# Kernel tuning notes

Hardware: AMD Instinct MI355X
Metric: run time of the kernel (lower is better)

## Reference

```python
import jax, jax.numpy as jnp
import numpy as np

NNZ = 819200
NUM_SESS = 16384
ITEMS_NUM = 1000000
EMB_DIM = 64


def setup_inputs() -> dict:
    key = jax.random.key(0)
    k1, k2, k3, k4 = jax.random.split(key, 4)
    row_idx = jnp.sort(jax.random.randint(k1, (NNZ,), 0, NUM_SESS, dtype=jnp.int32))
    col_idx = jax.random.randint(k2, (NNZ,), 0, ITEMS_NUM, dtype=jnp.int32)
    data_tensor = jax.random.uniform(k3, (NNZ,), dtype=jnp.float32)
    embeddings = jax.random.normal(k4, (ITEMS_NUM, EMB_DIM), dtype=jnp.float32)
    return {
        "row_idx": row_idx,
        "col_idx": col_idx,
        "data_tensor": data_tensor,
        "num_ids": NUM_SESS,
        "embeddings": embeddings,
    }


def reference(row_idx, col_idx, data_tensor, num_ids, embeddings):
    # sparse_coo([num_ids, ITEMS_NUM]) @ embeddings
    # == per-session weighted sum of gathered item embeddings.
    gathered = embeddings[col_idx]                      # [nnz, d]
    weighted = gathered * data_tensor[:, None]          # [nnz, d]
    user_embeddings = jax.ops.segment_sum(
        weighted, row_idx, num_segments=num_ids)        # [num_ids, d]
    return user_embeddings
```

## Files before the change

kernel.cpp:

```cpp
#include <hip/hip_runtime.h>


__global__ __launch_bounds__(256) void build_rowptr_kernel(
    const int* __restrict__ row_idx,
    int*       __restrict__ row_ptr,
    int nnz, int num_sess)
{
    int j = blockIdx.x * blockDim.x + threadIdx.x;
    if (j >= nnz) return;
    int r = row_idx[j];
    if (j == 0) {
        for (int s = 0; s <= r; ++s) row_ptr[s] = 0;
    } else {
        int rp = row_idx[j - 1];
        for (int s = rp + 1; s <= r; ++s) row_ptr[s] = j;
    }
    if (j == nnz - 1) {
        for (int s = r + 1; s <= num_sess; ++s) row_ptr[s] = nnz;
    }
}

__global__ __launch_bounds__(256, 8) void wsum_sess_kernel(
    const int*    __restrict__ row_ptr,
    const int*    __restrict__ col_idx,
    const float*  __restrict__ data,
    const float4* __restrict__ emb,
    float4*       __restrict__ out,
    int num_sess)
{
    const int wave = threadIdx.x >> 6;
    const int lane = threadIdx.x & 63;
    const int sess = (blockIdx.x << 2) + wave;
    if (sess >= num_sess) return;

    const int start = row_ptr[sess];
    const int end   = row_ptr[sess + 1];

    const int r = lane >> 4;
    const int c = lane & 15;

    float4 acc = make_float4(0.f, 0.f, 0.f, 0.f);

    int j0 = start;
    for (; j0 + 16 <= end; j0 += 16) {
        int   c0 = col_idx[j0 + 0  + r];
        int   c1 = col_idx[j0 + 4  + r];
        int   c2 = col_idx[j0 + 8  + r];
        int   c3 = col_idx[j0 + 12 + r];
        float w0 = data[j0 + 0  + r];
        float w1 = data[j0 + 4  + r];
        float w2 = data[j0 + 8  + r];
        float w3 = data[j0 + 12 + r];
        float4 e0 = emb[((size_t)c0 << 4) + c];
        float4 e1 = emb[((size_t)c1 << 4) + c];
        float4 e2 = emb[((size_t)c2 << 4) + c];
        float4 e3 = emb[((size_t)c3 << 4) + c];
        acc.x += w0 * e0.x + w1 * e1.x + w2 * e2.x + w3 * e3.x;
        acc.y += w0 * e0.y + w1 * e1.y + w2 * e2.y + w3 * e3.y;
        acc.z += w0 * e0.z + w1 * e1.z + w2 * e2.z + w3 * e3.z;
        acc.w += w0 * e0.w + w1 * e1.w + w2 * e2.w + w3 * e3.w;
    }
    for (; j0 < end; j0 += 4) {
        int   j     = j0 + r;
        bool  valid = (j < end);
        int   col   = valid ? col_idx[j] : 0;
        float w     = valid ? data[j]    : 0.f;
        float4 e = emb[((size_t)col << 4) + c];
        acc.x += w * e.x;
        acc.y += w * e.y;
        acc.z += w * e.z;
        acc.w += w * e.w;
    }

    acc.x += __shfl_xor(acc.x, 16, 64);
    acc.y += __shfl_xor(acc.y, 16, 64);
    acc.z += __shfl_xor(acc.z, 16, 64);
    acc.w += __shfl_xor(acc.w, 16, 64);
    acc.x += __shfl_xor(acc.x, 32, 64);
    acc.y += __shfl_xor(acc.y, 32, 64);
    acc.z += __shfl_xor(acc.z, 32, 64);
    acc.w += __shfl_xor(acc.w, 32, 64);

    if (r == 0)
        out[((size_t)sess << 4) + c] = acc;
}

extern "C" void kernel_launch(void* const* d_in, const int* in_sizes, int n_in,
                              void* d_out, int out_size, void* d_ws, size_t ws_size,
                              hipStream_t stream) {
    const int*   row_idx = (const int*)  d_in[0];
    const int*   col_idx = (const int*)  d_in[1];
    const float* data    = (const float*)d_in[2];
    const float* emb     = (const float*)d_in[4];

    const int nnz      = in_sizes[0];
    const int num_sess = out_size / 64;

    int* row_ptr = (int*)d_ws;

    build_rowptr_kernel<<<(nnz + 255) / 256, 256, 0, stream>>>(
        row_idx, row_ptr, nnz, num_sess);

    const int blocks = (num_sess + 3) / 4;
    wsum_sess_kernel<<<blocks, 256, 0, stream>>>(
        row_ptr, col_idx, data, (const float4*)emb, (float4*)d_out,
        num_sess);
}
```

Measured before the change: 325.3 us.

## Map one embedding column per lane and broadcast indices via readlane

Restructures the per-session gather so each lane owns one of the 64 embedding dimensions. A wave loads up to 64 col/weight pairs cooperatively and broadcasts each one with readlane. Up to 32 row loads are issued in flight before the accumulation, which removes the cross-lane shuffle reduction. The tradeoffs are scalar float loads instead of float4 loads, and padding work of up to 32 rows for short sessions (about 50 nnz per session on average), which wastes bandwidth on invalid entries that point at row 0.

```diff
diff --git a/kernel.cpp b/kernel.cpp
--- a/kernel.cpp
+++ b/kernel.cpp
@@ -21,11 +21,11 @@
 }
 
 __global__ __launch_bounds__(256, 8) void wsum_sess_kernel(
-    const int*    __restrict__ row_ptr,
-    const int*    __restrict__ col_idx,
-    const float*  __restrict__ data,
-    const float4* __restrict__ emb,
-    float4*       __restrict__ out,
+    const int*   __restrict__ row_ptr,
+    const int*   __restrict__ col_idx,
+    const float* __restrict__ data,
+    const float* __restrict__ emb,
+    float*       __restrict__ out,
     int num_sess)
 {
     const int wave = threadIdx.x >> 6;
@@ -36,53 +36,34 @@
     const int start = row_ptr[sess];
     const int end   = row_ptr[sess + 1];
 
-    const int r = lane >> 4;
-    const int c = lane & 15;
+    float acc = 0.0f;
 
-    float4 acc = make_float4(0.f, 0.f, 0.f, 0.f);
+    for (int j0 = start; j0 < end; j0 += 64) {
+        const int jl    = j0 + lane;
+        const bool valid = (jl < end);
+        int   col = valid ? col_idx[jl] : 0;
+        float w   = valid ? data[jl]    : 0.0f;
+        const int rem = end - j0;
 
-    int j0 = start;
-    for (; j0 + 16 <= end; j0 += 16) {
-        int   c0 = col_idx[j0 + 0  + r];
-        int   c1 = col_idx[j0 + 4  + r];
-        int   c2 = col_idx[j0 + 8  + r];
-        int   c3 = col_idx[j0 + 12 + r];
-        float w0 = data[j0 + 0  + r];
-        float w1 = data[j0 + 4  + r];
-        float w2 = data[j0 + 8  + r];
-        float w3 = data[j0 + 12 + r];
-        float4 e0 = emb[((size_t)c0 << 4) + c];
-        float4 e1 = emb[((size_t)c1 << 4) + c];
-        float4 e2 = emb[((size_t)c2 << 4) + c];
-        float4 e3 = emb[((size_t)c3 << 4) + c];
-        acc.x += w0 * e0.x + w1 * e1.x + w2 * e2.x + w3 * e3.x;
-        acc.y += w0 * e0.y + w1 * e1.y + w2 * e2.y + w3 * e3.y;
-        acc.z += w0 * e0.z + w1 * e1.z + w2 * e2.z + w3 * e3.z;
-        acc.w += w0 * e0.w + w1 * e1.w + w2 * e2.w + w3 * e3.w;
-    }
-    for (; j0 < end; j0 += 4) {
-        int   j     = j0 + r;
-        bool  valid = (j < end);
-        int   col   = valid ? col_idx[j] : 0;
-        float w     = valid ? data[j]    : 0.f;
-        float4 e = emb[((size_t)col << 4) + c];
-        acc.x += w * e.x;
-        acc.y += w * e.y;
-        acc.z += w * e.z;
-        acc.w += w * e.w;
+        #pragma unroll
+        for (int kb = 0; kb < 64; kb += 32) {
+            if (kb >= rem) break;
+            float v[32];
+            float wk[32];
+            #pragma unroll
+            for (int k = 0; k < 32; ++k) {
+                int c = __builtin_amdgcn_readlane(col, kb + k);
+                wk[k] = __int_as_float(
+                            __builtin_amdgcn_readlane(__float_as_int(w), kb + k));
+                v[k] = emb[(size_t)c * 64 + lane];
+            }
+            #pragma unroll
+            for (int k = 0; k < 32; ++k)
+                acc += wk[k] * v[k];
+        }
     }
 
-    acc.x += __shfl_xor(acc.x, 16, 64);
-    acc.y += __shfl_xor(acc.y, 16, 64);
-    acc.z += __shfl_xor(acc.z, 16, 64);
-    acc.w += __shfl_xor(acc.w, 16, 64);
-    acc.x += __shfl_xor(acc.x, 32, 64);
-    acc.y += __shfl_xor(acc.y, 32, 64);
-    acc.z += __shfl_xor(acc.z, 32, 64);
-    acc.w += __shfl_xor(acc.w, 32, 64);
-
-    if (r == 0)
-        out[((size_t)sess << 4) + c] = acc;
+    out[(size_t)sess * 64 + lane] = acc;
 }
 
 extern "C" void kernel_launch(void* const* d_in, const int* in_sizes, int n_in,
@@ -103,6 +84,5 @@
 
     const int blocks = (num_sess + 3) / 4;
     wsum_sess_kernel<<<blocks, 256, 0, stream>>>(
-        row_ptr, col_idx, data, (const float4*)emb, (float4*)d_out,
-        num_sess);
+        row_ptr, col_idx, data, emb, (float*)d_out, num_sess);
 }
```

Measured after the change: 335.7 us. 3.2% more time.
